# Kernel optimization log

Measured on AMD Instinct MI355X. Metric: run time of the kernel, lower is better.

## Reference

```python
import jax, jax.numpy as jnp
import numpy as np

B, T, E = 4, 2048, 1024
H, KV = 16, 4          # query heads, key/value heads
D = E // H             # head_dim = 64
G = H // KV            # query heads per kv head = 4
NEG = -1e9


def setup_inputs() -> dict:
    key = jax.random.key(0)
    ks = jax.random.split(key, 6)
    hidden_states = jax.random.normal(ks[0], (B, T, E), dtype=jnp.float32)
    # additive causal mask [B, 1, T, T]
    causal = jnp.where(jnp.tril(jnp.ones((T, T), dtype=bool)), 0.0, NEG).astype(jnp.float32)
    attention_mask = jnp.broadcast_to(causal[None, None], (B, 1, T, T))
    s = 0.02
    Wq = jax.random.normal(ks[1], (E, E), dtype=jnp.float32) * s
    Wk = jax.random.normal(ks[2], (E, KV * D), dtype=jnp.float32) * s
    Wv = jax.random.normal(ks[3], (E, KV * D), dtype=jnp.float32) * s
    Wo = jax.random.normal(ks[4], (E, E), dtype=jnp.float32) * s
    bq = jnp.zeros((E,), jnp.float32)
    bk = jnp.zeros((KV * D,), jnp.float32)
    bv = jnp.zeros((KV * D,), jnp.float32)
    bo = jnp.zeros((E,), jnp.float32)
    return {"hidden_states": hidden_states, "attention_mask": attention_mask,
            "Wq": Wq, "bq": bq, "Wk": Wk, "bk": bk, "Wv": Wv, "bv": bv,
            "Wo": Wo, "bo": bo}


def reference(hidden_states, attention_mask, Wq, bq, Wk, bk, Wv, bv, Wo, bo):
    b, t, e = hidden_states.shape
    scaling = D ** -0.5
    # projections (torch Linear: x @ W + b with W stored [in, out])
    q = (hidden_states @ Wq + bq) * scaling           # [b, t, E]
    k = hidden_states @ Wk + bk                        # [b, t, KV*D]
    v = hidden_states @ Wv + bv
    # [b, KV, G, t, D] for q; [b, KV, t, D] for k/v (GQA grouping == repeat_kv math)
    q = q.reshape(b, t, KV, G, D).transpose(0, 2, 3, 1, 4)
    k = k.reshape(b, t, KV, D).transpose(0, 2, 1, 3)
    v = v.reshape(b, t, KV, D).transpose(0, 2, 1, 3)
    scores = jnp.einsum('bkgsd,bktd->bkgst', q, k)     # [b, KV, G, t, t]
    scores = scores + attention_mask[:, :, None, :, :]  # broadcast [b,1,1,t,t]
    w = jax.nn.softmax(scores, axis=-1)
    out = jnp.einsum('bkgst,bktd->bkgsd', w, v)        # [b, KV, G, t, D]
    out = out.transpose(0, 3, 1, 2, 4).reshape(b, t, e)  # heads back to embed
    return out @ Wo + bo
```

## Files before the change

kernel.cpp:

```cpp
#include <hip/hip_runtime.h>

typedef __bf16 bf16;
typedef __attribute__((ext_vector_type(8))) __bf16 bf16x8;
typedef __attribute__((ext_vector_type(4))) __bf16 bf16x4;
typedef __attribute__((ext_vector_type(4))) float f32x4;

#define B_ 4
#define T_ 2048
#define E_ 1024
#define H_ 16
#define KV_ 4
#define D_ 64
#define KVD_ 256
#define QKVS_ 1536
#define M_ 8192

#define MASK_NEG (-3.0e4f)
#define QSCALE (0.125f * 1.4426950408889634f)

__device__ inline bf16x8 load8(const bf16* p) { return *(const bf16x8*)p; }
__device__ inline bf16x8 load8(const float* p) {
  f32x4 a = *(const f32x4*)p;
  f32x4 b = *(const f32x4*)(p + 4);
  bf16x8 r;
#pragma unroll
  for (int j = 0; j < 4; ++j) { r[j] = (bf16)a[j]; r[4 + j] = (bf16)b[j]; }
  return r;
}

__device__ inline void gload_lds16(const bf16* g, bf16* l) {
  __builtin_amdgcn_global_load_lds(
      (const __attribute__((address_space(1))) void*)g,
      (__attribute__((address_space(3))) void*)l, 16, 0, 0);
}

__global__ __launch_bounds__(256) void cast_k(const float* __restrict__ src,
                                              bf16* __restrict__ dst) {
  size_t i = ((size_t)blockIdx.x * 256 + threadIdx.x) * 8;
  *(bf16x8*)(dst + i) = load8(src + i);
}

__global__ __launch_bounds__(256) void wprep_k(const float* __restrict__ Wq,
                                               const float* __restrict__ Wk,
                                               const float* __restrict__ Wv,
                                               const float* __restrict__ Wo,
                                               bf16* __restrict__ WqkvT,
                                               bf16* __restrict__ WoT) {
  const int z = blockIdx.z;
  const float* W;
  bf16* WT;
  int N;
  if (z == 0) { W = Wq; WT = WqkvT; N = 1024; }
  else if (z == 1) { W = Wo; WT = WoT; N = 1024; }
  else if (z == 2) { if (blockIdx.y >= 8) return; W = Wk; WT = WqkvT + 1024 * 1024; N = 256; }
  else { if (blockIdx.y >= 8) return; W = Wv; WT = WqkvT + 1280 * 1024; N = 256; }

  __shared__ bf16 tile[32][33];
  int k0 = blockIdx.x * 32, n0 = blockIdx.y * 32;
  int tr = threadIdx.x >> 5;
  int tc = threadIdx.x & 31;
#pragma unroll
  for (int i = 0; i < 32; i += 8)
    tile[tr + i][tc] = (bf16)W[(size_t)(k0 + tr + i) * N + n0 + tc];
  __syncthreads();
#pragma unroll
  for (int i = 0; i < 32; i += 8)
    WT[(size_t)(n0 + tr + i) * 1024 + k0 + tc] = tile[tc][tr + i];
}

__global__ __launch_bounds__(256) void vtrans_k(const bf16* __restrict__ src,
                                                bf16* __restrict__ dst) {
  __shared__ bf16 tile[32][33];
  int r0 = blockIdx.x * 32;
  int c0 = blockIdx.y * 32;
  int tr = threadIdx.x >> 5, tc = threadIdx.x & 31;
#pragma unroll
  for (int i = 0; i < 32; i += 8)
    tile[tr + i][tc] = src[(size_t)(r0 + tr + i) * QKVS_ + 1280 + c0 + tc];
  __syncthreads();
#pragma unroll
  for (int i = 0; i < 32; i += 8) {
    int c = c0 + tr + i;
    int r = r0 + tc;
    dst[(size_t)((r >> 11) * KVD_ + c) * T_ + (r & (T_ - 1))] = tile[tc][tr + i];
  }
}

__global__ __launch_bounds__(256) void qkv_gemm_k(const bf16* __restrict__ A,
                                                  const bf16* __restrict__ WT,
                                                  const float* __restrict__ bq,
                                                  const float* __restrict__ bk,
                                                  const float* __restrict__ bv,
                                                  bf16* __restrict__ C) {
  const int K = E_;
  const int m0 = blockIdx.x * 128;
  const int n0 = blockIdx.y * 128;
  const int tid = threadIdx.x;
  const int wave = tid >> 6;
  const int lane = tid & 63;
  const int wr = wave >> 1;
  const int wc = wave & 1;
  const int fr = lane & 15;
  const int quad = lane >> 4;

  __shared__ bf16 sA[128][32];
  __shared__ bf16 sB[128][32];

  f32x4 acc[4][4] = {};

  const int ldr = lane >> 2;
  const int ldk = (lane & 3) * 8;
  const bf16* Ag0 = A + (size_t)(m0 + wave * 32 + ldr) * K + ldk;
  const bf16* Ag1 = Ag0 + (size_t)16 * K;
  const bf16* Bg0 = WT + (size_t)(n0 + wave * 32 + ldr) * K + ldk;
  const bf16* Bg1 = Bg0 + (size_t)16 * K;
  bf16* sA0 = &sA[wave * 32][0];
  bf16* sA1 = &sA[wave * 32 + 16][0];
  bf16* sB0 = &sB[wave * 32][0];
  bf16* sB1 = &sB[wave * 32 + 16][0];

  for (int k0 = 0; k0 < K; k0 += 32) {
    gload_lds16(Ag0 + k0, sA0);
    gload_lds16(Ag1 + k0, sA1);
    gload_lds16(Bg0 + k0, sB0);
    gload_lds16(Bg1 + k0, sB1);
    __syncthreads();

    bf16x8 af[4], bfr[4];
#pragma unroll
    for (int m = 0; m < 4; ++m)
      af[m] = *(const bf16x8*)(&sA[wr * 64 + m * 16 + fr][quad * 8]);
#pragma unroll
    for (int n = 0; n < 4; ++n)
      bfr[n] = *(const bf16x8*)(&sB[wc * 64 + n * 16 + fr][quad * 8]);
#pragma unroll
    for (int m = 0; m < 4; ++m)
#pragma unroll
      for (int n = 0; n < 4; ++n)
        acc[m][n] = __builtin_amdgcn_mfma_f32_16x16x32_bf16(af[m], bfr[n], acc[m][n], 0, 0, 0);
    __syncthreads();
  }

#pragma unroll
  for (int n = 0; n < 4; ++n) {
    int col = n0 + wc * 64 + n * 16 + fr;
    float bias, sc;
    if (col < 1024) { bias = bq[col]; sc = QSCALE; }
    else if (col < 1280) { bias = bk[col - 1024]; sc = 1.f; }
    else { bias = bv[col - 1280]; sc = 1.f; }
#pragma unroll
    for (int m = 0; m < 4; ++m) {
#pragma unroll
      for (int i = 0; i < 4; ++i) {
        int row = m0 + wr * 64 + m * 16 + quad * 4 + i;
        C[(size_t)row * QKVS_ + col] = (bf16)((acc[m][n][i] + bias) * sc);
      }
    }
  }
}

__global__ __launch_bounds__(256) void gemm128_k(const bf16* __restrict__ A,
                                                 const bf16* __restrict__ WT,
                                                 const float* __restrict__ bias,
                                                 float* __restrict__ C,
                                                 int M, int N, int K) {
  const int m0 = blockIdx.x * 128;
  const int n0 = blockIdx.y * 128;
  const int tid = threadIdx.x;
  const int wave = tid >> 6;
  const int lane = tid & 63;
  const int wr = wave >> 1;
  const int wc = wave & 1;
  const int fr = lane & 15;
  const int quad = lane >> 4;

  __shared__ bf16 sA[128][32];
  __shared__ bf16 sB[128][32];

  f32x4 acc[4][4] = {};

  const int ldr = lane >> 2;
  const int ldk = (lane & 3) * 8;
  const bf16* Ag0 = A + (size_t)(m0 + wave * 32 + ldr) * K + ldk;
  const bf16* Ag1 = Ag0 + (size_t)16 * K;
  const bf16* Bg0 = WT + (size_t)(n0 + wave * 32 + ldr) * K + ldk;
  const bf16* Bg1 = Bg0 + (size_t)16 * K;
  bf16* sA0 = &sA[wave * 32][0];
  bf16* sA1 = &sA[wave * 32 + 16][0];
  bf16* sB0 = &sB[wave * 32][0];
  bf16* sB1 = &sB[wave * 32 + 16][0];

  for (int k0 = 0; k0 < K; k0 += 32) {
    gload_lds16(Ag0 + k0, sA0);
    gload_lds16(Ag1 + k0, sA1);
    gload_lds16(Bg0 + k0, sB0);
    gload_lds16(Bg1 + k0, sB1);
    __syncthreads();

    bf16x8 af[4], bfr[4];
#pragma unroll
    for (int m = 0; m < 4; ++m)
      af[m] = *(const bf16x8*)(&sA[wr * 64 + m * 16 + fr][quad * 8]);
#pragma unroll
    for (int n = 0; n < 4; ++n)
      bfr[n] = *(const bf16x8*)(&sB[wc * 64 + n * 16 + fr][quad * 8]);
#pragma unroll
    for (int m = 0; m < 4; ++m)
#pragma unroll
      for (int n = 0; n < 4; ++n)
        acc[m][n] = __builtin_amdgcn_mfma_f32_16x16x32_bf16(af[m], bfr[n], acc[m][n], 0, 0, 0);
    __syncthreads();
  }

#pragma unroll
  for (int n = 0; n < 4; ++n) {
    int col = n0 + wc * 64 + n * 16 + fr;
    float bv = bias[col];
#pragma unroll
    for (int m = 0; m < 4; ++m) {
#pragma unroll
      for (int i = 0; i < 4; ++i) {
        int row = m0 + wr * 64 + m * 16 + quad * 4 + i;
        C[(size_t)row * N + col] = (acc[m][n][i] + bv);
      }
    }
  }
}

__global__ __launch_bounds__(256) void attn_k(const bf16* __restrict__ QKVg,
                                              const bf16* __restrict__ VTg,
                                              bf16* __restrict__ Og) {
  const int jp = blockIdx.x;
  const int h = blockIdx.y;
  const int b = blockIdx.z;
  const int kv = h >> 2;
  const int tid = threadIdx.x;
  const int wave = tid >> 6;
  const int lane = tid & 63;
  const int fr = lane & 15;
  const int quad = lane >> 4;

  __shared__ bf16 Ks[64][72];
  __shared__ bf16 Vt[64][72];
  __shared__ bf16 Pt[64][72];

  const int skey = tid & 63;
  const int sdc = (tid >> 6) * 16;
  const int svd = tid >> 2;
  const int svk = (tid & 3) * 16;
  const bf16* kbase = QKVg + (size_t)(b * T_ + skey) * QKVS_ + 1024 + kv * 64 + sdc;
  const bf16* vbase = VTg + (size_t)((b * KV_ + kv) * D_ + svd) * T_ + svk;

  for (int ph = 0; ph < 2; ++ph) {
    const int qb = ph ? (31 - jp) : jp;

    bf16x8 qa0, qa1;
    {
      const bf16* qsrc = QKVg + (size_t)(b * T_ + qb * 64 + wave * 16 + fr) * QKVS_ + h * 64 + quad * 8;
      qa0 = *(const bf16x8*)(qsrc);
      qa1 = *(const bf16x8*)(qsrc + 32);
    }

    f32x4 Oacc[4] = {};
    float m_run = MASK_NEG, l_run = 0.f;

    bf16x8 k0p, k1p, v0p, v1p;
    k0p = *(const bf16x8*)(kbase);
    k1p = *(const bf16x8*)(kbase + 8);
    v0p = *(const bf16x8*)(vbase);
    v1p = *(const bf16x8*)(vbase + 8);

    for (int kb = 0; kb <= qb; ++kb) {
      *(bf16x8*)(&Ks[skey][sdc]) = k0p;
      *(bf16x8*)(&Ks[skey][sdc + 8]) = k1p;
      *(bf16x8*)(&Vt[svd][svk]) = v0p;
      *(bf16x8*)(&Vt[svd][svk + 8]) = v1p;
      __syncthreads();

      if (kb < qb) {
        const bf16* kp = kbase + (size_t)(kb + 1) * 64 * QKVS_;
        const bf16* vp = vbase + (size_t)(kb + 1) * 64;
        k0p = *(const bf16x8*)(kp);
        k1p = *(const bf16x8*)(kp + 8);
        v0p = *(const bf16x8*)(vp);
        v1p = *(const bf16x8*)(vp + 8);
      } else if (ph == 0) {
        k0p = *(const bf16x8*)(kbase);
        k1p = *(const bf16x8*)(kbase + 8);
        v0p = *(const bf16x8*)(vbase);
        v1p = *(const bf16x8*)(vbase + 8);
      }

      f32x4 S[4] = {};
      __builtin_amdgcn_s_setprio(1);
#pragma unroll
      for (int nt = 0; nt < 4; ++nt) {
        bf16x8 kf0 = *(const bf16x8*)(&Ks[nt * 16 + fr][quad * 8]);
        bf16x8 kf1 = *(const bf16x8*)(&Ks[nt * 16 + fr][32 + quad * 8]);
        S[nt] = __builtin_amdgcn_mfma_f32_16x16x32_bf16(kf0, qa0, S[nt], 0, 0, 0);
        S[nt] = __builtin_amdgcn_mfma_f32_16x16x32_bf16(kf1, qa1, S[nt], 0, 0, 0);
      }
      __builtin_amdgcn_s_setprio(0);

      if (kb == qb) {
        const int ql = wave * 16 + fr;
#pragma unroll
        for (int nt = 0; nt < 4; ++nt)
#pragma unroll
          for (int i = 0; i < 4; ++i)
            if (nt * 16 + quad * 4 + i > ql) S[nt][i] = MASK_NEG;
      }

      float pm = S[0][0];
#pragma unroll
      for (int nt = 0; nt < 4; ++nt)
#pragma unroll
        for (int i = 0; i < 4; ++i) pm = fmaxf(pm, S[nt][i]);
      pm = fmaxf(pm, __shfl_xor(pm, 16, 64));
      pm = fmaxf(pm, __shfl_xor(pm, 32, 64));
      if (pm > m_run) {
        float al = exp2f(m_run - pm);
        m_run = pm;
        l_run *= al;
#pragma unroll
        for (int dt = 0; dt < 4; ++dt)
#pragma unroll
          for (int i = 0; i < 4; ++i) Oacc[dt][i] *= al;
      }
      float ps = 0.f;
#pragma unroll
      for (int nt = 0; nt < 4; ++nt)
#pragma unroll
        for (int i = 0; i < 4; ++i) {
          float p = exp2f(S[nt][i] - m_run);
          S[nt][i] = p;
          ps += p;
        }
      ps += __shfl_xor(ps, 16, 64);
      ps += __shfl_xor(ps, 32, 64);
      l_run += ps;

#pragma unroll
      for (int nt = 0; nt < 4; ++nt) {
        bf16x4 w;
#pragma unroll
        for (int i = 0; i < 4; ++i) w[i] = (bf16)S[nt][i];
        *(bf16x4*)(&Pt[wave * 16 + fr][nt * 16 + quad * 4]) = w;
      }
      __threadfence_block();

      bf16x8 pb0 = *(const bf16x8*)(&Pt[wave * 16 + fr][quad * 8]);
      bf16x8 pb1 = *(const bf16x8*)(&Pt[wave * 16 + fr][32 + quad * 8]);
      __builtin_amdgcn_s_setprio(1);
#pragma unroll
      for (int dt = 0; dt < 4; ++dt) {
        bf16x8 vf0 = *(const bf16x8*)(&Vt[dt * 16 + fr][quad * 8]);
        bf16x8 vf1 = *(const bf16x8*)(&Vt[dt * 16 + fr][32 + quad * 8]);
        Oacc[dt] = __builtin_amdgcn_mfma_f32_16x16x32_bf16(vf0, pb0, Oacc[dt], 0, 0, 0);
        Oacc[dt] = __builtin_amdgcn_mfma_f32_16x16x32_bf16(vf1, pb1, Oacc[dt], 0, 0, 0);
      }
      __builtin_amdgcn_s_setprio(0);
      __syncthreads();
    }

    {
      float inv = 1.f / fmaxf(l_run, 1e-30f);
      bf16* dst = Og + (size_t)(b * T_ + qb * 64 + wave * 16 + fr) * E_ + h * 64;
#pragma unroll
      for (int dt = 0; dt < 4; ++dt) {
        bf16x4 o;
#pragma unroll
        for (int i = 0; i < 4; ++i) o[i] = (bf16)(Oacc[dt][i] * inv);
        *(bf16x4*)(dst + dt * 16 + quad * 4) = o;
      }
    }
  }
}

extern "C" void kernel_launch(void* const* d_in, const int* in_sizes, int n_in,
                              void* d_out, int out_size, void* d_ws, size_t ws_size,
                              hipStream_t stream) {
  (void)in_sizes; (void)n_in; (void)out_size; (void)ws_size;
  const float* hidden = (const float*)d_in[0];
  const float* Wq = (const float*)d_in[2];
  const float* bq = (const float*)d_in[3];
  const float* Wk = (const float*)d_in[4];
  const float* bk = (const float*)d_in[5];
  const float* Wv = (const float*)d_in[6];
  const float* bv = (const float*)d_in[7];
  const float* Wo = (const float*)d_in[8];
  const float* bo = (const float*)d_in[9];
  float* out = (float*)d_out;

  char* ws = (char*)d_ws;
  bf16* WqkvT = (bf16*)(ws);
  bf16* WoT   = (bf16*)(ws + (3u << 20));
  bf16* QKVb  = (bf16*)(ws + (5u << 20));
  bf16* Hb    = (bf16*)(ws + (29u << 20));
  bf16* Ab    = (bf16*)(ws + (29u << 20));
  bf16* VbT   = (bf16*)(ws + (45u << 20));

  cast_k<<<dim3(M_ * E_ / (256 * 8)), 256, 0, stream>>>(hidden, Hb);
  wprep_k<<<dim3(32, 32, 4), 256, 0, stream>>>(Wq, Wk, Wv, Wo, WqkvT, WoT);

  qkv_gemm_k<<<dim3(64, 12), 256, 0, stream>>>(Hb, WqkvT, bq, bk, bv, QKVb);

  vtrans_k<<<dim3(256, 8), 256, 0, stream>>>(QKVb, VbT);

  attn_k<<<dim3(16, 16, 4), 256, 0, stream>>>(QKVb, VbT, Ab);

  gemm128_k<<<dim3(64, 8), 256, 0, stream>>>(Ab, WoT, bo, out, M_, E_, E_);
}
```

Before: 285.6 us.

## Fuse V transpose into QKV GEMM and rework attention with 32x32 MFMA tiles

Removes the separate V-transpose kernel by writing V directly in transposed layout from the QKV GEMM epilogue. The attention kernel now handles 128-query blocks per workgroup using 32x32x16 MFMAs, an XOR-swizzled LDS layout for K and V, and permlane32 swaps that keep P in registers instead of round-tripping through LDS. It also remaps block indices so that heads sharing a KV group land on the same XCD, which should improve L2 reuse. Larger per-wave tiles raise register pressure and halve the grid size, which may reduce occupancy.

Result: slower. 311.7 us (+9.1%).

```diff
diff --git a/kernel.cpp b/kernel.cpp
--- a/kernel.cpp
+++ b/kernel.cpp
@@ -3,7 +3,10 @@
 typedef __bf16 bf16;
 typedef __attribute__((ext_vector_type(8))) __bf16 bf16x8;
 typedef __attribute__((ext_vector_type(4))) __bf16 bf16x4;
+typedef __attribute__((ext_vector_type(2))) __bf16 bf16x2;
 typedef __attribute__((ext_vector_type(4))) float f32x4;
+typedef __attribute__((ext_vector_type(16))) float f32x16;
+typedef __attribute__((ext_vector_type(4))) unsigned u32x4;
 
 #define B_ 4
 #define T_ 2048
@@ -32,6 +35,27 @@
   __builtin_amdgcn_global_load_lds(
       (const __attribute__((address_space(1))) void*)g,
       (__attribute__((address_space(3))) void*)l, 16, 0, 0);
+}
+
+__device__ inline unsigned pk2(float a, float b) {
+  bf16x2 t; t[0] = (bf16)a; t[1] = (bf16)b;
+  return __builtin_bit_cast(unsigned, t);
+}
+
+__device__ inline void plswap(unsigned& x, unsigned& y) {
+#if __has_builtin(__builtin_amdgcn_permlane32_swap)
+  auto r = __builtin_amdgcn_permlane32_swap((int)x, (int)y, false, false);
+  x = (unsigned)r[0]; y = (unsigned)r[1];
+#else
+  asm volatile("v_permlane32_swap_b32 %0, %1" : "+v"(x), "+v"(y));
+#endif
+}
+
+__device__ inline bf16* swzp(bf16* base, int row, int c8) {
+  return base + row * 64 + ((c8 ^ (row & 7)) << 3);
+}
+__device__ inline const bf16* swzr(const bf16* base, int row, int c8) {
+  return base + row * 64 + ((c8 ^ (row & 7)) << 3);
 }
 
 __global__ __launch_bounds__(256) void cast_k(const float* __restrict__ src,
@@ -68,30 +92,13 @@
     WT[(size_t)(n0 + tr + i) * 1024 + k0 + tc] = tile[tc][tr + i];
 }
 
-__global__ __launch_bounds__(256) void vtrans_k(const bf16* __restrict__ src,
-                                                bf16* __restrict__ dst) {
-  __shared__ bf16 tile[32][33];
-  int r0 = blockIdx.x * 32;
-  int c0 = blockIdx.y * 32;
-  int tr = threadIdx.x >> 5, tc = threadIdx.x & 31;
-#pragma unroll
-  for (int i = 0; i < 32; i += 8)
-    tile[tr + i][tc] = src[(size_t)(r0 + tr + i) * QKVS_ + 1280 + c0 + tc];
-  __syncthreads();
-#pragma unroll
-  for (int i = 0; i < 32; i += 8) {
-    int c = c0 + tr + i;
-    int r = r0 + tc;
-    dst[(size_t)((r >> 11) * KVD_ + c) * T_ + (r & (T_ - 1))] = tile[tc][tr + i];
-  }
-}
-
 __global__ __launch_bounds__(256) void qkv_gemm_k(const bf16* __restrict__ A,
                                                   const bf16* __restrict__ WT,
                                                   const float* __restrict__ bq,
                                                   const float* __restrict__ bk,
                                                   const float* __restrict__ bv,
-                                                  bf16* __restrict__ C) {
+                                                  bf16* __restrict__ C,
+                                                  bf16* __restrict__ VbT) {
   const int K = E_;
   const int m0 = blockIdx.x * 128;
   const int n0 = blockIdx.y * 128;
@@ -144,16 +151,29 @@
 #pragma unroll
   for (int n = 0; n < 4; ++n) {
     int col = n0 + wc * 64 + n * 16 + fr;
-    float bias, sc;
-    if (col < 1024) { bias = bq[col]; sc = QSCALE; }
-    else if (col < 1280) { bias = bk[col - 1024]; sc = 1.f; }
-    else { bias = bv[col - 1280]; sc = 1.f; }
-#pragma unroll
-    for (int m = 0; m < 4; ++m) {
-#pragma unroll
-      for (int i = 0; i < 4; ++i) {
-        int row = m0 + wr * 64 + m * 16 + quad * 4 + i;
-        C[(size_t)row * QKVS_ + col] = (bf16)((acc[m][n][i] + bias) * sc);
+    if (col < 1280) {
+      float bias, sc;
+      if (col < 1024) { bias = bq[col]; sc = QSCALE; }
+      else { bias = bk[col - 1024]; sc = 1.f; }
+#pragma unroll
+      for (int m = 0; m < 4; ++m) {
+#pragma unroll
+        for (int i = 0; i < 4; ++i) {
+          int row = m0 + wr * 64 + m * 16 + quad * 4 + i;
+          C[(size_t)row * QKVS_ + col] = (bf16)((acc[m][n][i] + bias) * sc);
+        }
+      }
+    } else {
+      float bias = bv[col - 1280];
+      int kvd = col - 1280;
+      bf16* vrow = VbT + ((size_t)((m0 >> 11) * 256 + kvd)) * T_ +
+                   (m0 & (T_ - 1)) + wr * 64 + quad * 4;
+#pragma unroll
+      for (int m = 0; m < 4; ++m) {
+        bf16x4 o;
+#pragma unroll
+        for (int i = 0; i < 4; ++i) o[i] = (bf16)(acc[m][n][i] + bias);
+        *(bf16x4*)(vrow + m * 16) = o;
       }
     }
   }
@@ -230,38 +250,44 @@
 __global__ __launch_bounds__(256) void attn_k(const bf16* __restrict__ QKVg,
                                               const bf16* __restrict__ VTg,
                                               bf16* __restrict__ Og) {
-  const int jp = blockIdx.x;
-  const int h = blockIdx.y;
-  const int b = blockIdx.z;
-  const int kv = h >> 2;
+  const int lin = blockIdx.x + 8 * blockIdx.y + 128 * blockIdx.z;
+  const int xcd = lin & 7;
+  const int idx = lin >> 3;
+  const int g = xcd + 8 * (idx >> 5);
+  const int t5 = idx & 31;
+  const int jp = t5 & 7;
+  const int hg = t5 >> 3;
+  const int b = g >> 2, kv = g & 3, h = kv * 4 + hg;
+
   const int tid = threadIdx.x;
   const int wave = tid >> 6;
   const int lane = tid & 63;
-  const int fr = lane & 15;
-  const int quad = lane >> 4;
-
-  __shared__ bf16 Ks[64][72];
-  __shared__ bf16 Vt[64][72];
-  __shared__ bf16 Pt[64][72];
-
-  const int skey = tid & 63;
-  const int sdc = (tid >> 6) * 16;
-  const int svd = tid >> 2;
-  const int svk = (tid & 3) * 16;
-  const bf16* kbase = QKVg + (size_t)(b * T_ + skey) * QKVS_ + 1024 + kv * 64 + sdc;
-  const bf16* vbase = VTg + (size_t)((b * KV_ + kv) * D_ + svd) * T_ + svk;
+  const int col = lane & 31;
+  const int hi = lane >> 5;
+
+  __shared__ bf16 Ks[64 * 64];
+  __shared__ bf16 Vt[64 * 64];
+
+  const int srow = tid & 63;
+  const int seg = tid >> 6;
+  const bf16* kbase = QKVg + (size_t)(b * T_ + srow) * QKVS_ + 1024 + kv * 64 + seg * 16;
+  const bf16* vbase = VTg + (size_t)((b * KV_ + kv) * D_ + srow) * T_ + seg * 16;
+  bf16* kd0 = swzp(Ks, srow, 2 * seg);
+  bf16* kd1 = swzp(Ks, srow, 2 * seg + 1);
+  bf16* vd0 = swzp(Vt, srow, 2 * seg);
+  bf16* vd1 = swzp(Vt, srow, 2 * seg + 1);
 
   for (int ph = 0; ph < 2; ++ph) {
-    const int qb = ph ? (31 - jp) : jp;
-
-    bf16x8 qa0, qa1;
-    {
-      const bf16* qsrc = QKVg + (size_t)(b * T_ + qb * 64 + wave * 16 + fr) * QKVS_ + h * 64 + quad * 8;
-      qa0 = *(const bf16x8*)(qsrc);
-      qa1 = *(const bf16x8*)(qsrc + 32);
-    }
-
-    f32x4 Oacc[4] = {};
+    const int qb = ph ? (15 - jp) : jp;
+    const int qglob = qb * 128 + wave * 32 + col;
+
+    const bf16* qsrc = QKVg + (size_t)(b * T_ + qglob) * QKVS_ + h * 64 + hi * 8;
+    bf16x8 Qf0 = *(const bf16x8*)(qsrc);
+    bf16x8 Qf1 = *(const bf16x8*)(qsrc + 16);
+    bf16x8 Qf2 = *(const bf16x8*)(qsrc + 32);
+    bf16x8 Qf3 = *(const bf16x8*)(qsrc + 48);
+
+    f32x16 O0 = {}, O1 = {};
     float m_run = MASK_NEG, l_run = 0.f;
 
     bf16x8 k0p, k1p, v0p, v1p;
@@ -270,16 +296,17 @@
     v0p = *(const bf16x8*)(vbase);
     v1p = *(const bf16x8*)(vbase + 8);
 
-    for (int kb = 0; kb <= qb; ++kb) {
-      *(bf16x8*)(&Ks[skey][sdc]) = k0p;
-      *(bf16x8*)(&Ks[skey][sdc + 8]) = k1p;
-      *(bf16x8*)(&Vt[svd][svk]) = v0p;
-      *(bf16x8*)(&Vt[svd][svk + 8]) = v1p;
+    const int kbmax = 2 * qb + 1;
+    for (int kb = 0; kb <= kbmax; ++kb) {
+      *(bf16x8*)kd0 = k0p;
+      *(bf16x8*)kd1 = k1p;
+      *(bf16x8*)vd0 = v0p;
+      *(bf16x8*)vd1 = v1p;
       __syncthreads();
 
-      if (kb < qb) {
+      if (kb < kbmax) {
         const bf16* kp = kbase + (size_t)(kb + 1) * 64 * QKVS_;
-        const bf16* vp = vbase + (size_t)(kb + 1) * 64;
+        const bf16* vp = vbase + (kb + 1) * 64;
         k0p = *(const bf16x8*)(kp);
         k1p = *(const bf16x8*)(kp + 8);
         v0p = *(const bf16x8*)(vp);
@@ -291,73 +318,84 @@
         v1p = *(const bf16x8*)(vbase + 8);
       }
 
-      f32x4 S[4] = {};
+      f32x16 S0 = {}, S1 = {};
       __builtin_amdgcn_s_setprio(1);
 #pragma unroll
-      for (int nt = 0; nt < 4; ++nt) {
-        bf16x8 kf0 = *(const bf16x8*)(&Ks[nt * 16 + fr][quad * 8]);
-        bf16x8 kf1 = *(const bf16x8*)(&Ks[nt * 16 + fr][32 + quad * 8]);
-        S[nt] = __builtin_amdgcn_mfma_f32_16x16x32_bf16(kf0, qa0, S[nt], 0, 0, 0);
-        S[nt] = __builtin_amdgcn_mfma_f32_16x16x32_bf16(kf1, qa1, S[nt], 0, 0, 0);
+      for (int ks = 0; ks < 4; ++ks) {
+        bf16x8 kf0 = *(const bf16x8*)swzr(Ks, col, 2 * ks + hi);
+        bf16x8 kf1 = *(const bf16x8*)swzr(Ks, 32 + col, 2 * ks + hi);
+        bf16x8 qf = (ks == 0) ? Qf0 : (ks == 1) ? Qf1 : (ks == 2) ? Qf2 : Qf3;
+        S0 = __builtin_amdgcn_mfma_f32_32x32x16_bf16(kf0, qf, S0, 0, 0, 0);
+        S1 = __builtin_amdgcn_mfma_f32_32x32x16_bf16(kf1, qf, S1, 0, 0, 0);
       }
       __builtin_amdgcn_s_setprio(0);
 
-      if (kb == qb) {
-        const int ql = wave * 16 + fr;
-#pragma unroll
-        for (int nt = 0; nt < 4; ++nt)
-#pragma unroll
-          for (int i = 0; i < 4; ++i)
-            if (nt * 16 + quad * 4 + i > ql) S[nt][i] = MASK_NEG;
-      }
-
-      float pm = S[0][0];
-#pragma unroll
-      for (int nt = 0; nt < 4; ++nt)
-#pragma unroll
-        for (int i = 0; i < 4; ++i) pm = fmaxf(pm, S[nt][i]);
-      pm = fmaxf(pm, __shfl_xor(pm, 16, 64));
+      if (kb >= 2 * qb) {
+        const int qlcl = wave * 32 + col;
+        const int kbb = (kb - 2 * qb) * 64;
+#pragma unroll
+        for (int e = 0; e < 16; ++e) {
+          int row = (e & 3) + 8 * (e >> 2) + 4 * hi;
+          if (kbb + row > qlcl) S0[e] = MASK_NEG;
+          if (kbb + 32 + row > qlcl) S1[e] = MASK_NEG;
+        }
+      }
+
+      float pm = S0[0];
+#pragma unroll
+      for (int e = 1; e < 16; ++e) pm = fmaxf(pm, S0[e]);
+#pragma unroll
+      for (int e = 0; e < 16; ++e) pm = fmaxf(pm, S1[e]);
       pm = fmaxf(pm, __shfl_xor(pm, 32, 64));
       if (pm > m_run) {
         float al = exp2f(m_run - pm);
         m_run = pm;
         l_run *= al;
 #pragma unroll
-        for (int dt = 0; dt < 4; ++dt)
-#pragma unroll
-          for (int i = 0; i < 4; ++i) Oacc[dt][i] *= al;
+        for (int e = 0; e < 16; ++e) { O0[e] *= al; O1[e] *= al; }
       }
       float ps = 0.f;
 #pragma unroll
-      for (int nt = 0; nt < 4; ++nt)
-#pragma unroll
-        for (int i = 0; i < 4; ++i) {
-          float p = exp2f(S[nt][i] - m_run);
-          S[nt][i] = p;
-          ps += p;
-        }
-      ps += __shfl_xor(ps, 16, 64);
+      for (int e = 0; e < 16; ++e) { float p = exp2f(S0[e] - m_run); S0[e] = p; ps += p; }
+#pragma unroll
+      for (int e = 0; e < 16; ++e) { float p = exp2f(S1[e] - m_run); S1[e] = p; ps += p; }
       ps += __shfl_xor(ps, 32, 64);
       l_run += ps;
 
-#pragma unroll
-      for (int nt = 0; nt < 4; ++nt) {
-        bf16x4 w;
-#pragma unroll
-        for (int i = 0; i < 4; ++i) w[i] = (bf16)S[nt][i];
-        *(bf16x4*)(&Pt[wave * 16 + fr][nt * 16 + quad * 4]) = w;
-      }
-      __threadfence_block();
-
-      bf16x8 pb0 = *(const bf16x8*)(&Pt[wave * 16 + fr][quad * 8]);
-      bf16x8 pb1 = *(const bf16x8*)(&Pt[wave * 16 + fr][32 + quad * 8]);
+      bf16x8 P0, P1, P2, P3;
+      {
+        unsigned w0, w1, w2, w3;
+        u32x4 fv;
+        w0 = pk2(S0[0], S0[1]);  w1 = pk2(S0[2], S0[3]);
+        w2 = pk2(S0[4], S0[5]);  w3 = pk2(S0[6], S0[7]);
+        plswap(w0, w2); plswap(w1, w3);
+        fv[0] = w0; fv[1] = w1; fv[2] = w2; fv[3] = w3;
+        P0 = __builtin_bit_cast(bf16x8, fv);
+        w0 = pk2(S0[8], S0[9]);   w1 = pk2(S0[10], S0[11]);
+        w2 = pk2(S0[12], S0[13]); w3 = pk2(S0[14], S0[15]);
+        plswap(w0, w2); plswap(w1, w3);
+        fv[0] = w0; fv[1] = w1; fv[2] = w2; fv[3] = w3;
+        P1 = __builtin_bit_cast(bf16x8, fv);
+        w0 = pk2(S1[0], S1[1]);  w1 = pk2(S1[2], S1[3]);
+        w2 = pk2(S1[4], S1[5]);  w3 = pk2(S1[6], S1[7]);
+        plswap(w0, w2); plswap(w1, w3);
+        fv[0] = w0; fv[1] = w1; fv[2] = w2; fv[3] = w3;
+        P2 = __builtin_bit_cast(bf16x8, fv);
+        w0 = pk2(S1[8], S1[9]);   w1 = pk2(S1[10], S1[11]);
+        w2 = pk2(S1[12], S1[13]); w3 = pk2(S1[14], S1[15]);
+        plswap(w0, w2); plswap(w1, w3);
+        fv[0] = w0; fv[1] = w1; fv[2] = w2; fv[3] = w3;
+        P3 = __builtin_bit_cast(bf16x8, fv);
+      }
+
       __builtin_amdgcn_s_setprio(1);
 #pragma unroll
-      for (int dt = 0; dt < 4; ++dt) {
-        bf16x8 vf0 = *(const bf16x8*)(&Vt[dt * 16 + fr][quad * 8]);
-        bf16x8 vf1 = *(const bf16x8*)(&Vt[dt * 16 + fr][32 + quad * 8]);
-        Oacc[dt] = __builtin_amdgcn_mfma_f32_16x16x32_bf16(vf0, pb0, Oacc[dt], 0, 0, 0);
-        Oacc[dt] = __builtin_amdgcn_mfma_f32_16x16x32_bf16(vf1, pb1, Oacc[dt], 0, 0, 0);
+      for (int ksl = 0; ksl < 4; ++ksl) {
+        bf16x8 pf = (ksl == 0) ? P0 : (ksl == 1) ? P1 : (ksl == 2) ? P2 : P3;
+        bf16x8 vf0 = *(const bf16x8*)swzr(Vt, col, 2 * ksl + hi);
+        bf16x8 vf1 = *(const bf16x8*)swzr(Vt, 32 + col, 2 * ksl + hi);
+        O0 = __builtin_amdgcn_mfma_f32_32x32x16_bf16(vf0, pf, O0, 0, 0, 0);
+        O1 = __builtin_amdgcn_mfma_f32_32x32x16_bf16(vf1, pf, O1, 0, 0, 0);
       }
       __builtin_amdgcn_s_setprio(0);
       __syncthreads();
@@ -365,13 +403,17 @@
 
     {
       float inv = 1.f / fmaxf(l_run, 1e-30f);
-      bf16* dst = Og + (size_t)(b * T_ + qb * 64 + wave * 16 + fr) * E_ + h * 64;
-#pragma unroll
-      for (int dt = 0; dt < 4; ++dt) {
-        bf16x4 o;
-#pragma unroll
-        for (int i = 0; i < 4; ++i) o[i] = (bf16)(Oacc[dt][i] * inv);
-        *(bf16x4*)(dst + dt * 16 + quad * 4) = o;
+      bf16* dst = Og + (size_t)(b * T_ + qglob) * E_ + h * 64 + 4 * hi;
+#pragma unroll
+      for (int gg = 0; gg < 4; ++gg) {
+        bf16x4 o0, o1;
+#pragma unroll
+        for (int i = 0; i < 4; ++i) {
+          o0[i] = (bf16)(O0[4 * gg + i] * inv);
+          o1[i] = (bf16)(O1[4 * gg + i] * inv);
+        }
+        *(bf16x4*)(dst + 8 * gg) = o0;
+        *(bf16x4*)(dst + 32 + 8 * gg) = o1;
       }
     }
   }
@@ -403,11 +445,9 @@
   cast_k<<<dim3(M_ * E_ / (256 * 8)), 256, 0, stream>>>(hidden, Hb);
   wprep_k<<<dim3(32, 32, 4), 256, 0, stream>>>(Wq, Wk, Wv, Wo, WqkvT, WoT);
 
-  qkv_gemm_k<<<dim3(64, 12), 256, 0, stream>>>(Hb, WqkvT, bq, bk, bv, QKVb);
-
-  vtrans_k<<<dim3(256, 8), 256, 0, stream>>>(QKVb, VbT);
-
-  attn_k<<<dim3(16, 16, 4), 256, 0, stream>>>(QKVb, VbT, Ab);
+  qkv_gemm_k<<<dim3(64, 12), 256, 0, stream>>>(Hb, WqkvT, bq, bk, bv, QKVb, VbT);
+
+  attn_k<<<dim3(8, 16, 4), 256, 0, stream>>>(QKVb, VbT, Ab);
 
   gemm128_k<<<dim3(64, 8), 256, 0, stream>>>(Ab, WoT, bo, out, M_, E_, E_);
 }
```
